# Kernel tuning notes

Hardware: AMD Instinct MI355X
Metric: run time of the kernel (lower is better)

Reference implementation:

```python
import jax, jax.numpy as jnp
import numpy as np

B, S, H = 16, 128, 768
L, K = 2, 4
NORM_ITEM = 0.5


def _xavier(key, shape):
    fan_in, fan_out = shape[-1], shape[-2]
    std = float(np.sqrt(2.0 / (fan_in + fan_out)))
    return jax.random.normal(key, shape, dtype=jnp.float32) * std


def setup_inputs() -> dict:
    key = jax.random.key(0)
    ks = jax.random.split(key, 13)
    sentences = jax.random.normal(ks[0], (B, S, H), dtype=jnp.float32)
    adj_matrix = jax.random.uniform(ks[1], (B, K, S, S), dtype=jnp.float32)
    return {
        "sentences": sentences,
        "adj_matrix": adj_matrix,
        # stacked per-(layer, dep_kind) parameters
        "W_in": _xavier(ks[2], (L, K, H, H)),
        "b_in": _xavier(ks[3], (L, K, H, 1)),
        "W_out": _xavier(ks[4], (L, K, H, H)),
        "b_out": _xavier(ks[5], (L, K, H, 1)),
        "Wg_in": _xavier(ks[6], (L, K, H, H)),
        "bg_in": _xavier(ks[7], (L, K, H, 1)),
        "Wg_out": _xavier(ks[8], (L, K, H, H)),
        "bg_out": _xavier(ks[9], (L, K, H, 1)),
        "W_loop": _xavier(ks[10], (L, H, H)),
    }


def reference(sentences, adj_matrix, W_in, b_in, W_out, b_out,
              Wg_in, bg_in, Wg_out, bg_out, W_loop):
    # sentences: [B,S,H], adj_matrix: [B,K,S,S]
    adj_in = adj_matrix                       # message along edges
    adj_out = jnp.swapaxes(adj_matrix, 2, 3)  # reversed edges
    h = jnp.swapaxes(sentences, 1, 2)         # [B,H,S]

    def conv(Wg, bg, W, b, adj, h):
        # Wg,W: [K,H,H]; bg,b: [K,H,1]; adj: [B,K,S,S]; h: [B,H,S]
        gate = jax.nn.sigmoid(jnp.einsum('khd,bds->bkhs', Wg, h) + bg[None])
        rel = NORM_ITEM * gate * (jnp.einsum('khd,bds->bkhs', W, h) + b[None])
        # bmm with adjacency, then sum over dep kinds
        return jnp.einsum('bkhs,bkst->bht', rel, adj)

    n_layers = W_in.shape[0]
    for l in range(n_layers):
        s = jnp.einsum('hd,bds->bhs', W_loop[l], h)  # self loop
        s = s + conv(Wg_in[l], bg_in[l], W_in[l], b_in[l], adj_in, h)
        s = s + conv(Wg_out[l], bg_out[l], W_out[l], b_out[l], adj_out, h)
        h = jax.nn.relu(s)
    return jnp.swapaxes(h, 1, 2)  # [B,S,H]
```

## Files before the change

### kernel.cpp

```cpp
#include <hip/hip_runtime.h>
#include <stdint.h>

#define B_ 16
#define S_ 128
#define H_ 768
#define K_ 4
#define L_ 2
#define T_ (B_*S_)

typedef __attribute__((ext_vector_type(4))) float f32x4;
typedef __attribute__((ext_vector_type(8))) short s16x8;
typedef __bf16 bf16x8 __attribute__((ext_vector_type(8)));
typedef unsigned short u16;

__device__ inline u16 f2bf(float f) {
    union { float f; uint32_t u; } v; v.f = f;
    uint32_t u = v.u;
    return (u16)((u + 0x7fffu + ((u >> 16) & 1u)) >> 16);
}

__device__ inline ushort4 f2bf4(float4 v) {
    ushort4 r; r.x = f2bf(v.x); r.y = f2bf(v.y); r.z = f2bf(v.z); r.w = f2bf(v.w);
    return r;
}

template <typename T>
__device__ inline auto mfma16_impl(T a, T b, f32x4 c, int)
    -> decltype(__builtin_amdgcn_mfma_f32_16x16x32_bf16(a, b, c, 0, 0, 0)) {
    return __builtin_amdgcn_mfma_f32_16x16x32_bf16(a, b, c, 0, 0, 0);
}
template <typename T>
__device__ inline f32x4 mfma16_impl(T a, T b, f32x4 c, long) {
    return __builtin_amdgcn_mfma_f32_16x16x32_bf16(
        __builtin_bit_cast(bf16x8, a), __builtin_bit_cast(bf16x8, b), c, 0, 0, 0);
}
__device__ inline f32x4 mfma16(s16x8 a, s16x8 b, f32x4 c) {
    return mfma16_impl(a, b, c, 0);
}

__device__ inline void gload_lds16(const void* g, void* l) {
    __builtin_amdgcn_global_load_lds(
        (__attribute__((address_space(1))) void*)(g),
        (__attribute__((address_space(3))) void*)(l), 16, 0, 0);
}

__device__ inline void stage128(const char* gRow0, int rowStrideBytes, char* ldsBase, int tid) {
    const int lane = tid & 63;
    const int w = tid >> 6;
    const int lr = lane >> 3;
    #pragma unroll
    for (int j = 0; j < 2; ++j) {
        const int seg = w * 2 + j;
        const int row = seg * 8 + lr;
        const int sb = ((lane & 7) << 4) ^ ((row & 7) << 4);
        gload_lds16(gRow0 + (size_t)row * rowStrideBytes + sb,
                    ldsBase + seg * 1024);
    }
}

__device__ inline void stage_tile(const char* gbase, int rowStrideBytes, u16* lds, int tid) {
    const int lane = tid & 63;
    const int w = tid >> 6;
    const int lr = lane >> 3;
    const int cb = (lane & 7) << 4;
    #pragma unroll
    for (int j = 0; j < 4; ++j) {
        const int seg = j * 4 + w;
        const int row = seg * 8 + lr;
        const int sb = cb ^ ((row & 7) << 4);
        gload_lds16(gbase + (size_t)row * rowStrideBytes + sb, lds + seg * 512);
    }
}

__device__ inline void stage64(const char* gbase, int rowStrideBytes, char* lds, int tid) {
    const int lane = tid & 63;
    const int w = tid >> 6;
    const int lr = lane >> 3;
    const int cb = (lane & 7) << 4;
    #pragma unroll
    for (int j = 0; j < 2; ++j) {
        const int seg = j * 4 + w;
        const int row = seg * 8 + lr;
        const int sb = cb ^ ((row & 7) << 4);
        gload_lds16(gbase + (size_t)row * rowStrideBytes + sb, lds + seg * 1024);
    }
}

__device__ inline s16x8 read_frag(const u16* lds, int row, int colByte) {
    const int bir = colByte ^ ((row & 7) << 4);
    return *(const s16x8*)((const char*)lds + row * 128 + bir);
}

__global__ void prep_weights(const float* __restrict__ Wg_in, const float* __restrict__ Wg_out,
                             const float* __restrict__ W_in,  const float* __restrict__ W_out,
                             const float* __restrict__ W_loop, const float* __restrict__ sent,
                             u16* __restrict__ Wg_all, u16* __restrict__ W_all,
                             u16* __restrict__ Wl, u16* __restrict__ X0) {
    const int i4 = blockIdx.x * blockDim.x + threadIdx.x;
    const int NW4 = L_ * K_ * H_ * H_ / 4;
    const int KHH4 = K_ * H_ * H_ / 4;
    if (i4 < NW4) {
        const int l = i4 / KHH4;
        const int rem = i4 - l * KHH4;
        const int d0 = (l * 2) * KHH4 + rem;
        const int d1 = d0 + KHH4;
        ((ushort4*)Wg_all)[d0] = f2bf4(((const float4*)Wg_in)[i4]);
        ((ushort4*)Wg_all)[d1] = f2bf4(((const float4*)Wg_out)[i4]);
        ((ushort4*)W_all)[d0]  = f2bf4(((const float4*)W_in)[i4]);
        ((ushort4*)W_all)[d1]  = f2bf4(((const float4*)W_out)[i4]);
    }
    if (i4 < L_ * H_ * H_ / 4)  ((ushort4*)Wl)[i4] = f2bf4(((const float4*)W_loop)[i4]);
    if (i4 < T_ * H_ / 4)       ((ushort4*)X0)[i4] = f2bf4(((const float4*)sent)[i4]);
}

__global__ void prep_adj(const float* __restrict__ adj, u16* __restrict__ adjA) {
    const int idx = blockIdx.x * blockDim.x + threadIdx.x;
    const int s = idx & 127;
    const int t = (idx >> 7) & 127;
    const int b = (idx >> 14) & 15;
    const int p = idx >> 18;
    const int dir = p >> 2, k = p & 3;
    const float v = dir ? adj[(((size_t)b * K_ + k) * S_ + t) * S_ + s]
                        : adj[(((size_t)b * K_ + k) * S_ + s) * S_ + t];
    adjA[idx] = f2bf(v);
}

__global__ __launch_bounds__(512, 2)
void gemm1_kernel(const u16* __restrict__ Xb,
                  const u16* __restrict__ Wg_all, const u16* __restrict__ W_all,
                  const float* __restrict__ bg_in, const float* __restrict__ bg_out,
                  const float* __restrict__ b_in,  const float* __restrict__ b_out,
                  int layer, u16* __restrict__ Rel2) {
    __shared__ __align__(16) char smem[131072];

    const int tid = threadIdx.x;
    const int lane = tid & 63;
    const int w = tid >> 6;
    const int wm = w >> 2;
    const int wn = w & 3;
    const int l15 = lane & 15;
    const int hi16 = (lane >> 4) << 4;

    const int bid = blockIdx.x;
    const int task = (bid & 7) * 48 + (bid >> 3);
    const int p = task / 48;
    const int r = task % 48;
    const int y = r >> 3;
    const int m = r & 7;
    const int m0 = m * 256;
    const int n0 = y * 128;
    const int dir = p >> 2, kk = p & 3;

    const size_t woff = ((size_t)(layer * 2 + dir) * K_ + kk) * (size_t)(H_ * H_);
    const char* gA  = (const char*)Xb + (size_t)m0 * (H_ * 2);
    const char* gBr = (const char*)(W_all + woff)  + (size_t)n0 * (H_ * 2);
    const char* gBg = (const char*)(Wg_all + woff) + (size_t)n0 * (H_ * 2);

    auto STAGE = [&](int kt, int c) {
        char* base = smem + c * 65536;
        stage128(gA + (size_t)kt * 128, H_ * 2, base, tid);
        stage128(gA + (size_t)128 * (H_ * 2) + (size_t)kt * 128, H_ * 2, base + 16384, tid);
        stage128(gBr + (size_t)kt * 128, H_ * 2, base + 32768, tid);
        stage128(gBg + (size_t)kt * 128, H_ * 2, base + 49152, tid);
    };

    const f32x4 zf = {0.f, 0.f, 0.f, 0.f};
    f32x4 accr[8][2], accg[8][2];
    #pragma unroll
    for (int i = 0; i < 8; ++i)
        #pragma unroll
        for (int j = 0; j < 2; ++j) { accr[i][j] = zf; accg[i][j] = zf; }

    STAGE(0, 0);
    __syncthreads();

    for (int t = 0; t < 12; ++t) {
        const int c = t & 1;
        if (t < 11) STAGE(t + 1, c ^ 1);
        const u16* lA  = (const u16*)(smem + c * 65536);
        const u16* lBr = (const u16*)(smem + c * 65536 + 32768);
        const u16* lBg = (const u16*)(smem + c * 65536 + 49152);
        #pragma unroll
        for (int kq = 0; kq < 2; ++kq) {
            const int ck = kq * 64 + hi16;
            s16x8 a[8], br[2], bg[2];
            #pragma unroll
            for (int i = 0; i < 8; ++i)
                a[i] = read_frag(lA, wm * 128 + i * 16 + l15, ck);
            #pragma unroll
            for (int j = 0; j < 2; ++j) {
                br[j] = read_frag(lBr, wn * 32 + j * 16 + l15, ck);
                bg[j] = read_frag(lBg, wn * 32 + j * 16 + l15, ck);
            }
            #pragma unroll
            for (int i = 0; i < 8; ++i) {
                #pragma unroll
                for (int j = 0; j < 2; ++j) {
                    accr[i][j] = mfma16(a[i], br[j], accr[i][j]);
                    accg[i][j] = mfma16(a[i], bg[j], accg[i][j]);
                }
            }
        }
        __syncthreads();
    }

    const float* bgp = (dir ? bg_out : bg_in) + ((size_t)layer * K_ + kk) * H_;
    const float* brp = (dir ? b_out  : b_in ) + ((size_t)layer * K_ + kk) * H_;
    #pragma unroll
    for (int j = 0; j < 2; ++j) {
        const int h = n0 + wn * 32 + j * 16 + l15;
        const float bgv = bgp[h];
        const float brv = brp[h];
        #pragma unroll
        for (int i = 0; i < 8; ++i) {
            const int tl = wm * 128 + i * 16 + ((lane >> 4) << 2);
            const int bidx = m * 2 + (tl >> 7);
            const int s0 = tl & 127;
            u16 tmp[4];
            #pragma unroll
            for (int rr = 0; rr < 4; ++rr) {
                const float g = accg[i][j][rr] + bgv;
                const float v = accr[i][j][rr] + brv;
                tmp[rr] = f2bf(0.5f * v / (1.f + __expf(-g)));
            }
            ushort4 pk; pk.x = tmp[0]; pk.y = tmp[1]; pk.z = tmp[2]; pk.w = tmp[3];
            *(ushort4*)(Rel2 + (((size_t)p * B_ + bidx) * H_ + h) * S_ + s0) = pk;
        }
    }
}

__global__ __launch_bounds__(256, 2)
void gemm2_kernel(const u16* __restrict__ adjA, const u16* __restrict__ Rel2,
                  const u16* __restrict__ Xc, const u16* __restrict__ Wlb,
                  int layer,
                  u16* __restrict__ Xn, float* __restrict__ Out, int lastLayer) {
    __shared__ __align__(16) char smem2[49152];

    const int tid = threadIdx.x;
    const int lane = tid & 63;
    const int w = tid >> 6;
    const int wm = w >> 1, wn = w & 1;
    const int l15 = lane & 15;
    const int hi16 = (lane >> 4) << 4;
    const int h0 = blockIdx.x * 64;
    const int b = blockIdx.y;

    const char* gX  = (const char*)Xc + ((size_t)b * S_) * (H_ * 2);
    const char* gWl = (const char*)(Wlb + (size_t)layer * H_ * H_) + (size_t)h0 * (H_ * 2);

    auto STAGE = [&](int q, int c) {
        char* base = smem2 + c * 24576;
        if (q < 12) {
            stage_tile(gX + (size_t)q * 128, H_ * 2, (u16*)base, tid);
            stage64(gWl + (size_t)q * 128, H_ * 2, base + 16384, tid);
        } else {
            const int qa = q - 12;
            const int p = qa >> 1, sc = qa & 1;
            const char* Ab = (const char*)adjA + ((size_t)p * B_ + b) * (S_ * S_ * 2) + sc * 128;
            const char* Bb = (const char*)Rel2 + (((size_t)p * B_ + b) * H_ + h0) * (S_ * 2) + sc * 128;
            stage_tile(Ab, S_ * 2, (u16*)base, tid);
            stage64(Bb, S_ * 2, base + 16384, tid);
        }
    };

    const f32x4 zf = {0.f, 0.f, 0.f, 0.f};
    f32x4 acc[4][2];
    #pragma unroll
    for (int i = 0; i < 4; ++i)
        #pragma unroll
        for (int j = 0; j < 2; ++j) acc[i][j] = zf;

    STAGE(0, 0);
    __syncthreads();

    for (int q = 0; q < 28; ++q) {
        const int c = q & 1;
        if (q < 27) STAGE(q + 1, c ^ 1);
        const u16* lA = (const u16*)(smem2 + c * 24576);
        const u16* lB = (const u16*)(smem2 + c * 24576 + 16384);
        #pragma unroll
        for (int kq = 0; kq < 2; ++kq) {
            const int ck = kq * 64 + hi16;
            s16x8 a[4], bb[2];
            #pragma unroll
            for (int i = 0; i < 4; ++i)
                a[i] = read_frag(lA, wm * 64 + i * 16 + l15, ck);
            #pragma unroll
            for (int j = 0; j < 2; ++j)
                bb[j] = read_frag(lB, wn * 32 + j * 16 + l15, ck);
            #pragma unroll
            for (int i = 0; i < 4; ++i)
                #pragma unroll
                for (int j = 0; j < 2; ++j)
                    acc[i][j] = mfma16(a[i], bb[j], acc[i][j]);
        }
        __syncthreads();
    }

    #pragma unroll
    for (int i = 0; i < 4; ++i) {
        const int tl = wm * 64 + i * 16 + ((lane >> 4) << 2);
        #pragma unroll
        for (int j = 0; j < 2; ++j) {
            const int h = h0 + wn * 32 + j * 16 + l15;
            #pragma unroll
            for (int rr = 0; rr < 4; ++rr) {
                const size_t t = (size_t)b * S_ + tl + rr;
                float v = fmaxf(acc[i][j][rr], 0.f);
                if (lastLayer) Out[t * H_ + h] = v;
                else           Xn[t * H_ + h] = f2bf(v);
            }
        }
    }
}

extern "C" void kernel_launch(void* const* d_in, const int* in_sizes, int n_in,
                              void* d_out, int out_size, void* d_ws, size_t ws_size,
                              hipStream_t stream) {
    const float* sent   = (const float*)d_in[0];
    const float* adj    = (const float*)d_in[1];
    const float* W_in   = (const float*)d_in[2];
    const float* b_in   = (const float*)d_in[3];
    const float* W_out  = (const float*)d_in[4];
    const float* b_out  = (const float*)d_in[5];
    const float* Wg_in  = (const float*)d_in[6];
    const float* bg_in  = (const float*)d_in[7];
    const float* Wg_out = (const float*)d_in[8];
    const float* bg_out = (const float*)d_in[9];
    const float* W_loop = (const float*)d_in[10];

    char* ws = (char*)d_ws;
    u16* Wg_all = (u16*)(ws);
    u16* W_all  = (u16*)(ws + 18874368);
    u16* Wlb    = (u16*)(ws + 37748736);
    u16* adjA   = (u16*)(ws + 40108032);
    u16* X0     = (u16*)(ws + 44302336);
    u16* X1     = (u16*)(ws + 47448064);
    u16* Rel2   = (u16*)(ws + 50593792);

    prep_weights<<<4608, 256, 0, stream>>>(Wg_in, Wg_out, W_in, W_out, W_loop, sent,
                                           Wg_all, W_all, Wlb, X0);
    prep_adj<<<8192, 256, 0, stream>>>(adj, adjA);

    u16* Xc = X0;
    u16* Xn = X1;
    for (int l = 0; l < L_; ++l) {
        gemm1_kernel<<<384, 512, 0, stream>>>(Xc, Wg_all, W_all,
                                              bg_in, bg_out, b_in, b_out,
                                              l, Rel2);
        gemm2_kernel<<<dim3(12, 16), 256, 0, stream>>>(adjA, Rel2, Xc, Wlb, l,
                                                       Xn, (float*)d_out, l == L_ - 1);
        u16* t = Xc; Xc = Xn; Xn = t;
    }
}
```

Baseline: 161.7 us.

## Shrink gemm1 tiles to 128x128 and run 3 tiles per block over 256 blocks

```diff
diff --git a/kernel.cpp b/kernel.cpp
--- a/kernel.cpp
+++ b/kernel.cpp
@@ -131,7 +131,7 @@
                   const float* __restrict__ bg_in, const float* __restrict__ bg_out,
                   const float* __restrict__ b_in,  const float* __restrict__ b_out,
                   int layer, u16* __restrict__ Rel2) {
-    __shared__ __align__(16) char smem[131072];
+    __shared__ __align__(16) char smem[98304];
 
     const int tid = threadIdx.x;
     const int lane = tid & 63;
@@ -142,89 +142,99 @@
     const int hi16 = (lane >> 4) << 4;
 
     const int bid = blockIdx.x;
-    const int task = (bid & 7) * 48 + (bid >> 3);
-    const int p = task / 48;
-    const int r = task % 48;
-    const int y = r >> 3;
-    const int m = r & 7;
-    const int m0 = m * 256;
-    const int n0 = y * 128;
+    const int p = bid & 7;
+    const int g = bid >> 3;
     const int dir = p >> 2, kk = p & 3;
-
     const size_t woff = ((size_t)(layer * 2 + dir) * K_ + kk) * (size_t)(H_ * H_);
-    const char* gA  = (const char*)Xb + (size_t)m0 * (H_ * 2);
-    const char* gBr = (const char*)(W_all + woff)  + (size_t)n0 * (H_ * 2);
-    const char* gBg = (const char*)(Wg_all + woff) + (size_t)n0 * (H_ * 2);
-
-    auto STAGE = [&](int kt, int c) {
-        char* base = smem + c * 65536;
-        stage128(gA + (size_t)kt * 128, H_ * 2, base, tid);
-        stage128(gA + (size_t)128 * (H_ * 2) + (size_t)kt * 128, H_ * 2, base + 16384, tid);
-        stage128(gBr + (size_t)kt * 128, H_ * 2, base + 32768, tid);
-        stage128(gBg + (size_t)kt * 128, H_ * 2, base + 49152, tid);
+
+    const char* gAt[3];
+    const char* gBrt[3];
+    const char* gBgt[3];
+    int ys[3], ms[3];
+    #pragma unroll
+    for (int i = 0; i < 3; ++i) {
+        const int task = g * 3 + i;
+        const int y = task / 16, m = task % 16;
+        ys[i] = y; ms[i] = m;
+        gAt[i]  = (const char*)Xb + (size_t)(m * 128) * (H_ * 2);
+        gBrt[i] = (const char*)(W_all + woff)  + (size_t)(y * 128) * (H_ * 2);
+        gBgt[i] = (const char*)(Wg_all + woff) + (size_t)(y * 128) * (H_ * 2);
+    }
+
+    const float* bgp = (dir ? bg_out : bg_in) + ((size_t)layer * K_ + kk) * H_;
+    const float* brp = (dir ? b_out  : b_in ) + ((size_t)layer * K_ + kk) * H_;
+
+    auto STAGE = [&](int i, int kt, int c) {
+        char* base = smem + c * 49152;
+        stage128(gAt[i]  + (size_t)kt * 128, H_ * 2, base, tid);
+        stage128(gBrt[i] + (size_t)kt * 128, H_ * 2, base + 16384, tid);
+        stage128(gBgt[i] + (size_t)kt * 128, H_ * 2, base + 32768, tid);
     };
 
     const f32x4 zf = {0.f, 0.f, 0.f, 0.f};
-    f32x4 accr[8][2], accg[8][2];
-    #pragma unroll
-    for (int i = 0; i < 8; ++i)
+    f32x4 accr[4][2], accg[4][2];
+    #pragma unroll
+    for (int i = 0; i < 4; ++i)
         #pragma unroll
         for (int j = 0; j < 2; ++j) { accr[i][j] = zf; accg[i][j] = zf; }
 
-    STAGE(0, 0);
+    STAGE(0, 0, 0);
     __syncthreads();
 
-    for (int t = 0; t < 12; ++t) {
-        const int c = t & 1;
-        if (t < 11) STAGE(t + 1, c ^ 1);
-        const u16* lA  = (const u16*)(smem + c * 65536);
-        const u16* lBr = (const u16*)(smem + c * 65536 + 32768);
-        const u16* lBg = (const u16*)(smem + c * 65536 + 49152);
-        #pragma unroll
-        for (int kq = 0; kq < 2; ++kq) {
-            const int ck = kq * 64 + hi16;
-            s16x8 a[8], br[2], bg[2];
-            #pragma unroll
-            for (int i = 0; i < 8; ++i)
-                a[i] = read_frag(lA, wm * 128 + i * 16 + l15, ck);
-            #pragma unroll
-            for (int j = 0; j < 2; ++j) {
-                br[j] = read_frag(lBr, wn * 32 + j * 16 + l15, ck);
-                bg[j] = read_frag(lBg, wn * 32 + j * 16 + l15, ck);
-            }
-            #pragma unroll
-            for (int i = 0; i < 8; ++i) {
+    #pragma unroll
+    for (int ti = 0; ti < 3; ++ti) {
+        for (int kt = 0; kt < 12; ++kt) {
+            const int c = kt & 1;
+            if (kt < 11)      STAGE(ti, kt + 1, c ^ 1);
+            else if (ti < 2)  STAGE(ti + 1, 0, c ^ 1);
+            const u16* lA  = (const u16*)(smem + c * 49152);
+            const u16* lBr = (const u16*)(smem + c * 49152 + 16384);
+            const u16* lBg = (const u16*)(smem + c * 49152 + 32768);
+            #pragma unroll
+            for (int kq = 0; kq < 2; ++kq) {
+                const int ck = kq * 64 + hi16;
+                s16x8 a[4], br[2], bg[2];
+                #pragma unroll
+                for (int i = 0; i < 4; ++i)
+                    a[i] = read_frag(lA, wm * 64 + i * 16 + l15, ck);
                 #pragma unroll
                 for (int j = 0; j < 2; ++j) {
-                    accr[i][j] = mfma16(a[i], br[j], accr[i][j]);
-                    accg[i][j] = mfma16(a[i], bg[j], accg[i][j]);
+                    br[j] = read_frag(lBr, wn * 32 + j * 16 + l15, ck);
+                    bg[j] = read_frag(lBg, wn * 32 + j * 16 + l15, ck);
+                }
+                #pragma unroll
+                for (int i = 0; i < 4; ++i) {
+                    #pragma unroll
+                    for (int j = 0; j < 2; ++j) {
+                        accr[i][j] = mfma16(a[i], br[j], accr[i][j]);
+                        accg[i][j] = mfma16(a[i], bg[j], accg[i][j]);
+                    }
                 }
             }
-        }
-        __syncthreads();
-    }
-
-    const float* bgp = (dir ? bg_out : bg_in) + ((size_t)layer * K_ + kk) * H_;
-    const float* brp = (dir ? b_out  : b_in ) + ((size_t)layer * K_ + kk) * H_;
-    #pragma unroll
-    for (int j = 0; j < 2; ++j) {
-        const int h = n0 + wn * 32 + j * 16 + l15;
-        const float bgv = bgp[h];
-        const float brv = brp[h];
-        #pragma unroll
-        for (int i = 0; i < 8; ++i) {
-            const int tl = wm * 128 + i * 16 + ((lane >> 4) << 2);
-            const int bidx = m * 2 + (tl >> 7);
-            const int s0 = tl & 127;
-            u16 tmp[4];
-            #pragma unroll
-            for (int rr = 0; rr < 4; ++rr) {
-                const float g = accg[i][j][rr] + bgv;
-                const float v = accr[i][j][rr] + brv;
-                tmp[rr] = f2bf(0.5f * v / (1.f + __expf(-g)));
+            __syncthreads();
+        }
+        {
+            const int y = ys[ti], m = ms[ti];
+            #pragma unroll
+            for (int j = 0; j < 2; ++j) {
+                const int h = y * 128 + wn * 32 + j * 16 + l15;
+                const float bgv = bgp[h];
+                const float brv = brp[h];
+                #pragma unroll
+                for (int i = 0; i < 4; ++i) {
+                    const int tl = wm * 64 + i * 16 + ((lane >> 4) << 2);
+                    u16 tmp[4];
+                    #pragma unroll
+                    for (int rr = 0; rr < 4; ++rr) {
+                        const float gv = accg[i][j][rr] + bgv;
+                        const float vv = accr[i][j][rr] + brv;
+                        tmp[rr] = f2bf(0.5f * vv / (1.f + __expf(-gv)));
+                    }
+                    ushort4 pk; pk.x = tmp[0]; pk.y = tmp[1]; pk.z = tmp[2]; pk.w = tmp[3];
+                    *(ushort4*)(Rel2 + (((size_t)p * B_ + m) * H_ + h) * S_ + tl) = pk;
+                    accr[i][j] = zf; accg[i][j] = zf;
+                }
             }
-            ushort4 pk; pk.x = tmp[0]; pk.y = tmp[1]; pk.z = tmp[2]; pk.w = tmp[3];
-            *(ushort4*)(Rel2 + (((size_t)p * B_ + bidx) * H_ + h) * S_ + s0) = pk;
         }
     }
 }
@@ -345,7 +355,7 @@
     u16* Xc = X0;
     u16* Xn = X1;
     for (int l = 0; l < L_; ++l) {
-        gemm1_kernel<<<384, 512, 0, stream>>>(Xc, Wg_all, W_all,
+        gemm1_kernel<<<256, 512, 0, stream>>>(Xc, Wg_all, W_all,
                                               bg_in, bg_out, b_in, b_out,
                                               l, Rel2);
         gemm2_kernel<<<dim3(12, 16), 256, 0, stream>>>(adjA, Rel2, Xc, Wlb, l,
```

Measured after the change: 153.3 us (median of 2 runs). 1.05x faster.
